# Performance work log

Measured on AMD Instinct MI355X. Metric: run time of the kernel, lower is better.

The kernel has to match this reference:

```python
import jax, jax.numpy as jnp
import numpy as np

B, S, E = 2, 2048, 1024
N_HEADS = 16
HEAD_DIM = E // N_HEADS  # 64
ATTN_SCALE = 1.0 / np.sqrt(E)  # NOTE: original scales by 1/sqrt(hidden_dim_phi), not head_dim
ROPE_BASE = 10000.0


def _rope(t):
    # t: (B, H, S, D) with D = HEAD_DIM; interleaved-pair RoPE (torchtune-style)
    d = t.shape[-1]
    s = t.shape[-2]
    inv_freq = 1.0 / (ROPE_BASE ** (jnp.arange(0, d, 2, dtype=jnp.float32) / d))  # (D/2,)
    ang = jnp.arange(s, dtype=jnp.float32)[:, None] * inv_freq[None, :]  # (S, D/2)
    cos, sin = jnp.cos(ang), jnp.sin(ang)  # (S, D/2)
    tp = t.reshape(t.shape[:-1] + (d // 2, 2))
    te, to = tp[..., 0], tp[..., 1]  # (B,H,S,D/2)
    oe = te * cos - to * sin
    oo = te * sin + to * cos
    return jnp.stack([oe, oo], axis=-1).reshape(t.shape)


def setup_inputs() -> dict:
    key = jax.random.key(0)
    ks = jax.random.split(key, 5)
    std = 0.02
    return {
        "x": jax.random.normal(ks[0], (B, S, E), dtype=jnp.float32),
        "W_q": jax.random.normal(ks[1], (E, E), dtype=jnp.float32) * std,
        "W_k": jax.random.normal(ks[2], (E, E), dtype=jnp.float32) * std,
        "W_v": jax.random.normal(ks[3], (E, E), dtype=jnp.float32) * std,
        "W_o": jax.random.normal(ks[4], (E, E), dtype=jnp.float32) * std,
    }


def reference(x, W_q, W_k, W_v, W_o):
    b, s, e = x.shape
    hd = e // N_HEADS
    # projections -> (B, H, S, D)
    def proj(w):
        return (x @ w).reshape(b, s, N_HEADS, hd).transpose(0, 2, 1, 3)
    q = _rope(proj(W_q))
    k = _rope(proj(W_k))
    v = proj(W_v)
    scores = jnp.einsum('bhsd,bhtd->bhst', q, k) * ATTN_SCALE  # (B,H,S,S)
    causal = jnp.triu(jnp.ones((s, s), dtype=bool), k=1)
    scores = jnp.where(causal, -jnp.inf, scores)
    probs = jax.nn.softmax(scores, axis=-1)  # dropout is identity in eval mode
    out = jnp.einsum('bhst,bhtd->bhsd', probs, v)
    out = out.transpose(0, 2, 1, 3).reshape(b, s, e)
    return out @ W_o
```

## Files before the change

kernel.cpp:

```cpp
#include <hip/hip_runtime.h>
#include <hip/hip_bf16.h>

#define S_LEN 2048
#define E_DIM 1024
#define NH 16
#define HD 64
#define ATTN_SCALE 0.03125f
#define KVB 128

typedef __attribute__((ext_vector_type(8))) short short8;
typedef __attribute__((ext_vector_type(8))) unsigned short ushort8;
typedef __attribute__((ext_vector_type(4))) unsigned short ushort4_t;
typedef __attribute__((ext_vector_type(4))) float f32x4;
typedef __attribute__((ext_vector_type(4))) float f4;

__device__ __forceinline__ float bf2f(unsigned short u) {
    unsigned int x = ((unsigned int)u) << 16;
    return __builtin_bit_cast(float, x);
}
__device__ __forceinline__ unsigned short f2bf(float f) {
    unsigned int x = __builtin_bit_cast(unsigned int, f);
    x += 0x7FFFu + ((x >> 16) & 1u);
    return (unsigned short)(x >> 16);
}
__device__ __forceinline__ void gload16(const unsigned short* g, unsigned short* l) {
    __builtin_amdgcn_global_load_lds(
        (__attribute__((address_space(1))) void*)g,
        (__attribute__((address_space(3))) void*)l, 16, 0, 0);
}

__global__ __launch_bounds__(256) void k_convert(const float* __restrict__ x,
                                                 unsigned short* __restrict__ xb) {
    size_t i = ((size_t)blockIdx.x * 256 + threadIdx.x) * 8;
    f4 a = *(const f4*)(x + i);
    f4 b = *(const f4*)(x + i + 4);
    ushort8 o;
    o[0] = f2bf(a[0]); o[1] = f2bf(a[1]); o[2] = f2bf(a[2]); o[3] = f2bf(a[3]);
    o[4] = f2bf(b[0]); o[5] = f2bf(b[1]); o[6] = f2bf(b[2]); o[7] = f2bf(b[3]);
    *(ushort8*)(xb + i) = o;
}

__global__ __launch_bounds__(256) void k_transw(const float* W0, const float* W1,
                                                const float* W2, const float* W3,
                                                unsigned short* T0, unsigned short* T1,
                                                unsigned short* T2, unsigned short* T3) {
    const float* W; unsigned short* T;
    switch (blockIdx.z) {
        case 0: W = W0; T = T0; break;
        case 1: W = W1; T = T1; break;
        case 2: W = W2; T = T2; break;
        default: W = W3; T = T3; break;
    }
    __shared__ float tile[32][33];
    int tx = threadIdx.x, ty = threadIdx.y;
    int bx = blockIdx.x * 32, by = blockIdx.y * 32;
#pragma unroll
    for (int i = 0; i < 4; i++)
        tile[ty + i * 8][tx] = W[(size_t)(by + ty + i * 8) * E_DIM + bx + tx];
    __syncthreads();
#pragma unroll
    for (int i = 0; i < 4; i++)
        T[(size_t)(bx + ty + i * 8) * E_DIM + by + tx] = f2bf(tile[tx][ty + i * 8]);
}

__global__ __launch_bounds__(256) void k_rope_table(float* __restrict__ cosT,
                                                    float* __restrict__ sinT) {
    int idx = blockIdx.x * 256 + threadIdx.x;
    int s = idx >> 5, j = idx & 31;
    float inv = expf(-(float)j * (9.210340371976184f / 32.f));
    float ang = (float)s * inv;
    cosT[idx] = cosf(ang);
    sinT[idx] = sinf(ang);
}

template <int BM, int BN, int NBN, bool QKV3>
__global__ __launch_bounds__(256, 3)
void k_gemmN(const unsigned short* __restrict__ A,
             const unsigned short* __restrict__ B,
             unsigned short* __restrict__ Qo,
             unsigned short* __restrict__ Ko,
             unsigned short* __restrict__ Vto,
             float* __restrict__ Fo,
             const float* __restrict__ cosT,
             const float* __restrict__ sinT) {
    constexpr int THREADS = 256;
    constexpr int WM = BM / 2, WN = BN / 2;
    constexpr int FM = WM / 16, FN = WN / 16;
    constexpr int NT = E_DIM / 64;
    constexpr int AR = BM * 8 / THREADS;
    constexpr int BR = BN * 8 / THREADS;
    constexpr int STG = AR + BR;
    constexpr int NWG = (4096 / BM) * NBN;
    __shared__ unsigned short Al[2][BM * 64];
    __shared__ unsigned short Bl[2][BN * 64];
    int tid = threadIdx.x, lane = tid & 63, wid = tid >> 6;
    int l15 = lane & 15, lg = lane >> 4;
    int wr = wid >> 1, wc = wid & 1;
    int orig = blockIdx.y * NBN + blockIdx.x;
    int wg = (orig & 7) * (NWG / 8) + (orig >> 3);
    int bm = wg / NBN, bn = wg % NBN;

    auto stage = [&](int buf, int k0) {
#pragma unroll
        for (int i = 0; i < AR; i++) {
            int r = i * (THREADS / 8) + wid * 8 + (lane >> 3);
            int cs = (lane & 7) ^ (r & 7);
            gload16(A + (size_t)(bm * BM + r) * E_DIM + k0 + cs * 8,
                    &Al[buf][i * (THREADS * 8) + wid * 512]);
        }
#pragma unroll
        for (int i = 0; i < BR; i++) {
            int r = i * (THREADS / 8) + wid * 8 + (lane >> 3);
            int cs = (lane & 7) ^ (r & 7);
            gload16(B + (size_t)(bn * BN + r) * E_DIM + k0 + cs * 8,
                    &Bl[buf][i * (THREADS * 8) + wid * 512]);
        }
    };

    f32x4 acc[FM][FN] = {};
    stage(0, 0);
    for (int t = 0; t < NT; t++) {
        int cur = t & 1;
        if (t + 1 < NT) {
            stage(cur ^ 1, (t + 1) * 64);
            asm volatile("s_waitcnt vmcnt(%0)" :: "n"(STG) : "memory");
        } else {
            asm volatile("s_waitcnt vmcnt(0)" ::: "memory");
        }
        __builtin_amdgcn_s_barrier();
        __builtin_amdgcn_sched_barrier(0);
#pragma unroll
        for (int ks = 0; ks < 2; ks++) {
            short8 af[FM], bfv[FN];
#pragma unroll
            for (int m = 0; m < FM; m++) {
                int r = wr * WM + m * 16 + l15;
                int gc = ks * 4 + lg;
                af[m] = *(const short8*)&Al[cur][r * 64 + ((gc ^ (r & 7)) << 3)];
            }
#pragma unroll
            for (int n = 0; n < FN; n++) {
                int r = wc * WN + n * 16 + l15;
                int gc = ks * 4 + lg;
                bfv[n] = *(const short8*)&Bl[cur][r * 64 + ((gc ^ (r & 7)) << 3)];
            }
            __builtin_amdgcn_s_setprio(1);
#pragma unroll
            for (int m = 0; m < FM; m++)
#pragma unroll
                for (int n = 0; n < FN; n++)
                    acc[m][n] = __builtin_amdgcn_mfma_f32_16x16x32_bf16(
                        af[m], bfv[n], acc[m][n], 0, 0, 0);
            __builtin_amdgcn_s_setprio(0);
        }
        __builtin_amdgcn_s_barrier();
    }
#pragma unroll
    for (int m = 0; m < FM; m++) {
        int r0 = bm * BM + wr * WM + m * 16 + lg * 4;
#pragma unroll
        for (int n = 0; n < FN; n++) {
            int colg = bn * BN + wc * WN + n * 16 + l15;
            if (QKV3) {
                int z = colg >> 10, c1 = colg & 1023;
                if (z == 2) {
                    int h = c1 >> 6, d = c1 & 63;
                    int bb = r0 >> 11, s = r0 & 2047;
                    ushort4_t p;
#pragma unroll
                    for (int r = 0; r < 4; r++) p[r] = f2bf(acc[m][n][r]);
                    *(ushort4_t*)(Vto + (((size_t)((bb * 16 + h) * 64 + d)) << 11) + s) = p;
                } else {
                    unsigned short* T = z ? Ko : Qo;
                    int dl = c1 & 63, j = dl >> 1;
                    float sgn = (dl & 1) ? 1.f : -1.f;
                    float scq = z ? 1.f : ATTN_SCALE;
#pragma unroll
                    for (int r = 0; r < 4; r++) {
                        int row = r0 + r, s = row & 2047;
                        float c = cosT[s * 32 + j], sn = sinT[s * 32 + j];
                        float v = acc[m][n][r];
                        float p = __shfl_xor(v, 1);
                        T[(size_t)row * E_DIM + c1] = f2bf((v * c + sgn * p * sn) * scq);
                    }
                }
            } else {
#pragma unroll
                for (int r = 0; r < 4; r++)
                    Fo[(size_t)(r0 + r) * E_DIM + colg] = acc[m][n][r];
            }
        }
    }
}

__global__ __launch_bounds__(256, 2) void k_attn(const unsigned short* __restrict__ Q,
                                                 const unsigned short* __restrict__ K,
                                                 const unsigned short* __restrict__ Vt,
                                                 unsigned short* __restrict__ O) {
    __shared__ unsigned short K_lds[128 * 64];
    __shared__ unsigned short V_lds[64 * 128];
    __shared__ unsigned short P_lds[4][16][136];
    int tid = threadIdx.x, lane = tid & 63, wid = tid >> 6;
    int l15 = lane & 15, lg = lane >> 4;
    int orig = blockIdx.y * 16 + blockIdx.x;
    int wg = (orig & 7) * 64 + (orig >> 3);
    int jp = wg & 15, bh = wg >> 4;
    int b = bh >> 4, h = bh & 15;
    const size_t base_qk = (size_t)b * S_LEN * E_DIM + (size_t)h * HD;
    const unsigned short* Vbh = Vt + ((size_t)(bh * 64) << 11);

    auto stageK = [&](int kt) {
        const unsigned short* Kb = K + base_qk + (size_t)(kt * KVB) * E_DIM;
#pragma unroll
        for (int i = 0; i < 4; i++) {
            int r = i * 32 + wid * 8 + (lane >> 3);
            int cs = (lane & 7) ^ (r & 7);
            gload16(Kb + (size_t)r * E_DIM + cs * 8, K_lds + i * 2048 + wid * 512);
        }
    };
    auto stageV = [&](int kt) {
#pragma unroll
        for (int i = 0; i < 4; i++) {
            int r = i * 16 + wid * 4 + (lane >> 4);
            int cs = (lane & 15) ^ (r & 7);
            gload16(Vbh + (size_t)r * 2048 + kt * KVB + cs * 8,
                    V_lds + i * 2048 + wid * 512);
        }
    };

    for (int pass = 0; pass < 2; ++pass) {
        int qt = pass ? (31 - jp) : jp;
        const unsigned short* Qb = Q + base_qk + (size_t)(qt * 64 + wid * 16) * E_DIM;
        short8 bq[2];
#pragma unroll
        for (int s2 = 0; s2 < 2; s2++)
            bq[s2] = *(const short8*)(Qb + (size_t)l15 * E_DIM + s2 * 32 + lg * 8);
        f32x4 acc_o[4] = {};
        float m_i = -1e30f, l_i = 0.f;
        int q_glob = qt * 64 + wid * 16 + l15;
        int nkt = (qt + 2) >> 1;
        stageK(0);
        stageV(0);
        asm volatile("s_waitcnt vmcnt(4)" ::: "memory");
        __builtin_amdgcn_s_barrier();
        __builtin_amdgcn_sched_barrier(0);
        for (int kt = 0; kt < nkt; ++kt) {
            f32x4 acc_s[8] = {};
            __builtin_amdgcn_s_setprio(1);
#pragma unroll
            for (int mf = 0; mf < 8; mf++) {
                int rK = mf * 16 + l15;
#pragma unroll
                for (int s2 = 0; s2 < 2; s2++) {
                    int gc = s2 * 4 + lg;
                    short8 a = *(const short8*)&K_lds[rK * 64 + ((gc ^ (rK & 7)) << 3)];
                    acc_s[mf] = __builtin_amdgcn_mfma_f32_16x16x32_bf16(
                        a, bq[s2], acc_s[mf], 0, 0, 0);
                }
            }
            __builtin_amdgcn_s_setprio(0);
            __builtin_amdgcn_s_barrier();
            if (kt + 1 < nkt) stageK(kt + 1);
            float sv[32];
            float vmax = -1e30f;
            if (kt == nkt - 1) {
#pragma unroll
                for (int mf = 0; mf < 8; mf++)
#pragma unroll
                    for (int r = 0; r < 4; r++) {
                        int kg = kt * KVB + mf * 16 + lg * 4 + r;
                        float v = acc_s[mf][r];
                        if (kg > q_glob) v = -1e30f;
                        sv[mf * 4 + r] = v;
                        vmax = fmaxf(vmax, v);
                    }
            } else {
#pragma unroll
                for (int mf = 0; mf < 8; mf++)
#pragma unroll
                    for (int r = 0; r < 4; r++) {
                        float v = acc_s[mf][r];
                        sv[mf * 4 + r] = v;
                        vmax = fmaxf(vmax, v);
                    }
            }
            vmax = fmaxf(vmax, __shfl_xor(vmax, 16));
            vmax = fmaxf(vmax, __shfl_xor(vmax, 32));
            float m_new = fmaxf(m_i, vmax);
            float corr = __expf(m_i - m_new);
            float rowsum = 0.f;
#pragma unroll
            for (int i = 0; i < 32; i++) {
                float p = __expf(sv[i] - m_new);
                sv[i] = p;
                rowsum += p;
            }
            rowsum += __shfl_xor(rowsum, 16);
            rowsum += __shfl_xor(rowsum, 32);
            l_i = l_i * corr + rowsum;
            m_i = m_new;
#pragma unroll
            for (int mf = 0; mf < 8; mf++) {
                ushort4_t pk;
#pragma unroll
                for (int r = 0; r < 4; r++) pk[r] = f2bf(sv[mf * 4 + r]);
                *(ushort4_t*)&P_lds[wid][l15][mf * 16 + lg * 4] = pk;
            }
#pragma unroll
            for (int r = 0; r < 4; r++) {
                float c4 = __shfl(corr, lg * 4 + r);
#pragma unroll
                for (int nf = 0; nf < 4; nf++) acc_o[nf][r] *= c4;
            }
            if (kt + 1 < nkt)
                asm volatile("s_waitcnt vmcnt(4)" ::: "memory");
            else
                asm volatile("s_waitcnt vmcnt(0)" ::: "memory");
            __builtin_amdgcn_s_barrier();
            __builtin_amdgcn_sched_barrier(0);
            __builtin_amdgcn_s_setprio(1);
#pragma unroll
            for (int s2 = 0; s2 < 4; s2++) {
                short8 pa = *(const short8*)&P_lds[wid][l15][s2 * 32 + lg * 8];
#pragma unroll
                for (int nf = 0; nf < 4; nf++) {
                    int rV = nf * 16 + l15;
                    int gc = s2 * 4 + lg;
                    short8 bv = *(const short8*)&V_lds[rV * 128 + ((gc ^ (rV & 7)) << 3)];
                    acc_o[nf] = __builtin_amdgcn_mfma_f32_16x16x32_bf16(
                        pa, bv, acc_o[nf], 0, 0, 0);
                }
            }
            __builtin_amdgcn_s_setprio(0);
            __builtin_amdgcn_s_barrier();
            if (kt + 1 < nkt) {
                stageV(kt + 1);
                asm volatile("s_waitcnt vmcnt(4)" ::: "memory");
            }
            __builtin_amdgcn_s_barrier();
            __builtin_amdgcn_sched_barrier(0);
        }
        unsigned short* Ob = O + base_qk + (size_t)(qt * 64 + wid * 16) * E_DIM;
#pragma unroll
        for (int r = 0; r < 4; r++) {
            float linv = 1.f / __shfl(l_i, lg * 4 + r);
#pragma unroll
            for (int nf = 0; nf < 4; nf++)
                Ob[(size_t)(lg * 4 + r) * E_DIM + nf * 16 + l15] =
                    f2bf(acc_o[nf][r] * linv);
        }
    }
}

extern "C" void kernel_launch(void* const* d_in, const int* in_sizes, int n_in,
                              void* d_out, int out_size, void* d_ws, size_t ws_size,
                              hipStream_t stream) {
    (void)in_sizes; (void)n_in; (void)out_size; (void)ws_size;
    const float* x  = (const float*)d_in[0];
    const float* Wq = (const float*)d_in[1];
    const float* Wk = (const float*)d_in[2];
    const float* Wv = (const float*)d_in[3];
    const float* Wo = (const float*)d_in[4];

    unsigned short* us = (unsigned short*)d_ws;
    unsigned short* xb    = us;
    unsigned short* WqkvT = us + 4194304;
    unsigned short* WoT   = us + 7340032;
    unsigned short* Qb    = us + 8388608;
    unsigned short* Kb    = us + 12582912;
    unsigned short* Vt    = us + 16777216;
    unsigned short* AO    = us + 20971520;
    float* cosT = (float*)((char*)d_ws + 50331648);
    float* sinT = cosT + 65536;

    k_convert<<<2048, 256, 0, stream>>>(x, xb);
    k_transw<<<dim3(32, 32, 4), dim3(32, 8), 0, stream>>>(
        Wq, Wk, Wv, Wo, WqkvT, WqkvT + 1048576, WqkvT + 2097152, WoT);
    k_rope_table<<<256, 256, 0, stream>>>(cosT, sinT);
    k_gemmN<128, 64, 48, true><<<dim3(48, 32), 256, 0, stream>>>(
        xb, WqkvT, Qb, Kb, Vt, nullptr, cosT, sinT);
    k_attn<<<dim3(16, 32), 256, 0, stream>>>(Qb, Kb, Vt, AO);
    k_gemmN<128, 64, 16, false><<<dim3(16, 32), 256, 0, stream>>>(
        AO, WoT, nullptr, nullptr, nullptr, (float*)d_out, cosT, sinT);
}
```

Before: 110.8 us.

## Double-buffer 64-wide KV tiles in attention with lazy rescale and exp2

Switches the attention kernel from single-buffered 128-key tiles staged between phases to double-buffered 64-key K/V tiles, prefetching the next tile at loop start and using one barrier per iteration. It also folds log2(e) into the Q scale so softmax uses exp2, skips the output rescale unless the running max grows by more than 8 (a lazy rescale), packs P with v_cvt_pk_bf16_f32, and raises launch bounds to 3 blocks per CU. This aims to cut barrier stalls and exp cost and to raise occupancy. In exchange the loop runs twice as many iterations, each doing less work.

```diff
diff --git a/kernel.cpp b/kernel.cpp
--- a/kernel.cpp
+++ b/kernel.cpp
@@ -6,13 +6,14 @@
 #define NH 16
 #define HD 64
 #define ATTN_SCALE 0.03125f
-#define KVB 128
+#define QSCALE_L2E 0.045084312f
 
 typedef __attribute__((ext_vector_type(8))) short short8;
 typedef __attribute__((ext_vector_type(8))) unsigned short ushort8;
 typedef __attribute__((ext_vector_type(4))) unsigned short ushort4_t;
 typedef __attribute__((ext_vector_type(4))) float f32x4;
 typedef __attribute__((ext_vector_type(4))) float f4;
+typedef __attribute__((ext_vector_type(2))) unsigned int uint2_t;
 
 __device__ __forceinline__ float bf2f(unsigned short u) {
     unsigned int x = ((unsigned int)u) << 16;
@@ -174,7 +175,7 @@
                     unsigned short* T = z ? Ko : Qo;
                     int dl = c1 & 63, j = dl >> 1;
                     float sgn = (dl & 1) ? 1.f : -1.f;
-                    float scq = z ? 1.f : ATTN_SCALE;
+                    float scq = z ? 1.f : QSCALE_L2E;
 #pragma unroll
                     for (int r = 0; r < 4; r++) {
                         int row = r0 + r, s = row & 2047;
@@ -193,13 +194,13 @@
     }
 }
 
-__global__ __launch_bounds__(256, 2) void k_attn(const unsigned short* __restrict__ Q,
+__global__ __launch_bounds__(256, 3) void k_attn(const unsigned short* __restrict__ Q,
                                                  const unsigned short* __restrict__ K,
                                                  const unsigned short* __restrict__ Vt,
                                                  unsigned short* __restrict__ O) {
-    __shared__ unsigned short K_lds[128 * 64];
-    __shared__ unsigned short V_lds[64 * 128];
-    __shared__ unsigned short P_lds[4][16][136];
+    __shared__ unsigned short K_lds[2][64 * 64];
+    __shared__ unsigned short V_lds[2][64 * 64];
+    __shared__ unsigned short P_lds[4][16][72];
     int tid = threadIdx.x, lane = tid & 63, wid = tid >> 6;
     int l15 = lane & 15, lg = lane >> 4;
     int orig = blockIdx.y * 16 + blockIdx.x;
@@ -209,22 +210,22 @@
     const size_t base_qk = (size_t)b * S_LEN * E_DIM + (size_t)h * HD;
     const unsigned short* Vbh = Vt + ((size_t)(bh * 64) << 11);
 
-    auto stageK = [&](int kt) {
-        const unsigned short* Kb = K + base_qk + (size_t)(kt * KVB) * E_DIM;
-#pragma unroll
-        for (int i = 0; i < 4; i++) {
-            int r = i * 32 + wid * 8 + (lane >> 3);
-            int cs = (lane & 7) ^ (r & 7);
-            gload16(Kb + (size_t)r * E_DIM + cs * 8, K_lds + i * 2048 + wid * 512);
+    auto stageK = [&](int buf, int kt) {
+#pragma unroll
+        for (int i = 0; i < 2; i++) {
+            int r = i * 32 + (tid >> 3);
+            int cs = (tid & 7) ^ (r & 7);
+            gload16(K + base_qk + (size_t)(kt * 64 + r) * E_DIM + cs * 8,
+                    &K_lds[buf][i * 2048 + tid * 8]);
         }
     };
-    auto stageV = [&](int kt) {
-#pragma unroll
-        for (int i = 0; i < 4; i++) {
-            int r = i * 16 + wid * 4 + (lane >> 4);
-            int cs = (lane & 15) ^ (r & 7);
-            gload16(Vbh + (size_t)r * 2048 + kt * KVB + cs * 8,
-                    V_lds + i * 2048 + wid * 512);
+    auto stageV = [&](int buf, int kt) {
+#pragma unroll
+        for (int i = 0; i < 2; i++) {
+            int r = i * 32 + (tid >> 3);
+            int cs = (tid & 7) ^ (r & 7);
+            gload16(Vbh + (size_t)r * 2048 + kt * 64 + cs * 8,
+                    &V_lds[buf][i * 2048 + tid * 8]);
         }
     };
 
@@ -238,37 +239,41 @@
         f32x4 acc_o[4] = {};
         float m_i = -1e30f, l_i = 0.f;
         int q_glob = qt * 64 + wid * 16 + l15;
-        int nkt = (qt + 2) >> 1;
-        stageK(0);
-        stageV(0);
-        asm volatile("s_waitcnt vmcnt(4)" ::: "memory");
+        int nkt = qt + 1;
+        stageK(0, 0);
+        stageV(0, 0);
+        asm volatile("s_waitcnt vmcnt(0)" ::: "memory");
         __builtin_amdgcn_s_barrier();
         __builtin_amdgcn_sched_barrier(0);
+        int cur = 0;
         for (int kt = 0; kt < nkt; ++kt) {
-            f32x4 acc_s[8] = {};
+            if (kt + 1 < nkt) {
+                stageK(cur ^ 1, kt + 1);
+                stageV(cur ^ 1, kt + 1);
+            }
+            f32x4 acc_s[4] = {};
             __builtin_amdgcn_s_setprio(1);
 #pragma unroll
-            for (int mf = 0; mf < 8; mf++) {
+            for (int mf = 0; mf < 4; mf++) {
                 int rK = mf * 16 + l15;
 #pragma unroll
                 for (int s2 = 0; s2 < 2; s2++) {
                     int gc = s2 * 4 + lg;
-                    short8 a = *(const short8*)&K_lds[rK * 64 + ((gc ^ (rK & 7)) << 3)];
+                    short8 a = *(const short8*)
+                        &K_lds[cur][rK * 64 + ((gc ^ (rK & 7)) << 3)];
                     acc_s[mf] = __builtin_amdgcn_mfma_f32_16x16x32_bf16(
                         a, bq[s2], acc_s[mf], 0, 0, 0);
                 }
             }
             __builtin_amdgcn_s_setprio(0);
-            __builtin_amdgcn_s_barrier();
-            if (kt + 1 < nkt) stageK(kt + 1);
-            float sv[32];
+            float sv[16];
             float vmax = -1e30f;
             if (kt == nkt - 1) {
 #pragma unroll
-                for (int mf = 0; mf < 8; mf++)
+                for (int mf = 0; mf < 4; mf++)
 #pragma unroll
                     for (int r = 0; r < 4; r++) {
-                        int kg = kt * KVB + mf * 16 + lg * 4 + r;
+                        int kg = kt * 64 + mf * 16 + lg * 4 + r;
                         float v = acc_s[mf][r];
                         if (kg > q_glob) v = -1e30f;
                         sv[mf * 4 + r] = v;
@@ -276,7 +281,7 @@
                     }
             } else {
 #pragma unroll
-                for (int mf = 0; mf < 8; mf++)
+                for (int mf = 0; mf < 4; mf++)
 #pragma unroll
                     for (int r = 0; r < 4; r++) {
                         float v = acc_s[mf][r];
@@ -286,59 +291,57 @@
             }
             vmax = fmaxf(vmax, __shfl_xor(vmax, 16));
             vmax = fmaxf(vmax, __shfl_xor(vmax, 32));
-            float m_new = fmaxf(m_i, vmax);
-            float corr = __expf(m_i - m_new);
+            if (!__all(vmax - m_i <= 8.0f)) {
+                float m_new = fmaxf(m_i, vmax);
+                float corr = exp2f(m_i - m_new);
+                l_i *= corr;
+#pragma unroll
+                for (int r = 0; r < 4; r++) {
+                    float c4 = __shfl(corr, lg * 4 + r);
+#pragma unroll
+                    for (int nf = 0; nf < 4; nf++) acc_o[nf][r] *= c4;
+                }
+                m_i = m_new;
+            }
             float rowsum = 0.f;
 #pragma unroll
-            for (int i = 0; i < 32; i++) {
-                float p = __expf(sv[i] - m_new);
+            for (int i = 0; i < 16; i++) {
+                float p = exp2f(sv[i] - m_i);
                 sv[i] = p;
                 rowsum += p;
             }
             rowsum += __shfl_xor(rowsum, 16);
             rowsum += __shfl_xor(rowsum, 32);
-            l_i = l_i * corr + rowsum;
-            m_i = m_new;
-#pragma unroll
-            for (int mf = 0; mf < 8; mf++) {
-                ushort4_t pk;
-#pragma unroll
-                for (int r = 0; r < 4; r++) pk[r] = f2bf(sv[mf * 4 + r]);
-                *(ushort4_t*)&P_lds[wid][l15][mf * 16 + lg * 4] = pk;
-            }
-#pragma unroll
-            for (int r = 0; r < 4; r++) {
-                float c4 = __shfl(corr, lg * 4 + r);
-#pragma unroll
-                for (int nf = 0; nf < 4; nf++) acc_o[nf][r] *= c4;
-            }
-            if (kt + 1 < nkt)
-                asm volatile("s_waitcnt vmcnt(4)" ::: "memory");
-            else
-                asm volatile("s_waitcnt vmcnt(0)" ::: "memory");
-            __builtin_amdgcn_s_barrier();
-            __builtin_amdgcn_sched_barrier(0);
+            l_i += rowsum;
+#pragma unroll
+            for (int mf = 0; mf < 4; mf++) {
+                unsigned int w0, w1;
+                asm("v_cvt_pk_bf16_f32 %0, %1, %2"
+                    : "=v"(w0) : "v"(sv[mf * 4 + 0]), "v"(sv[mf * 4 + 1]));
+                asm("v_cvt_pk_bf16_f32 %0, %1, %2"
+                    : "=v"(w1) : "v"(sv[mf * 4 + 2]), "v"(sv[mf * 4 + 3]));
+                uint2_t w; w[0] = w0; w[1] = w1;
+                *(uint2_t*)&P_lds[wid][l15][mf * 16 + lg * 4] = w;
+            }
             __builtin_amdgcn_s_setprio(1);
 #pragma unroll
-            for (int s2 = 0; s2 < 4; s2++) {
+            for (int s2 = 0; s2 < 2; s2++) {
                 short8 pa = *(const short8*)&P_lds[wid][l15][s2 * 32 + lg * 8];
 #pragma unroll
                 for (int nf = 0; nf < 4; nf++) {
                     int rV = nf * 16 + l15;
                     int gc = s2 * 4 + lg;
-                    short8 bv = *(const short8*)&V_lds[rV * 128 + ((gc ^ (rV & 7)) << 3)];
+                    short8 bv = *(const short8*)
+                        &V_lds[cur][rV * 64 + ((gc ^ (rV & 7)) << 3)];
                     acc_o[nf] = __builtin_amdgcn_mfma_f32_16x16x32_bf16(
                         pa, bv, acc_o[nf], 0, 0, 0);
                 }
             }
             __builtin_amdgcn_s_setprio(0);
-            __builtin_amdgcn_s_barrier();
-            if (kt + 1 < nkt) {
-                stageV(kt + 1);
-                asm volatile("s_waitcnt vmcnt(4)" ::: "memory");
-            }
+            asm volatile("s_waitcnt vmcnt(0)" ::: "memory");
             __builtin_amdgcn_s_barrier();
             __builtin_amdgcn_sched_barrier(0);
+            cur ^= 1;
         }
         unsigned short* Ob = O + base_qk + (size_t)(qt * 64 + wid * 16) * E_DIM;
 #pragma unroll
```

Result: slower. 117.5 us (+6.1%).
